# Kernel optimization log

Hardware: AMD Instinct MI355X
Metric: run time of the kernel (lower is better)

The kernel has to match this reference:

```python
import jax, jax.numpy as jnp
import numpy as np

H = 100; W = 100; FX = 86.6; FY = 86.6
NEAR = 2.0; FAR = 6.0; DINF = 1e10
NS = 64            # n_samples per ray
L_PTS = 10; L_DIR = 4
HID = 256; HID_DIR = 128
D_PTS = 3 + 3 * 2 * L_PTS   # 63
D_DIR = 3 + 3 * 2 * L_DIR   # 27


def posenc(x, L):
    # [x, sin(2^k x), cos(2^k x)] NeRF positional encoding
    freqs = (2.0 ** jnp.arange(L)).astype(x.dtype)          # [L]
    xb = x[..., None, :] * freqs[:, None]                    # [..., L, 3]
    enc = jnp.concatenate([jnp.sin(xb), jnp.cos(xb)], -1)    # [..., L, 6]
    return jnp.concatenate([x, enc.reshape(x.shape[:-1] + (L * 6,))], -1)


def setup_inputs() -> dict:
    key = jax.random.key(0)
    ks = jax.random.split(key, 8)
    pose = jnp.array([[1., 0., 0., 0.], [0., 1., 0., 0.],
                      [0., 0., 1., 4.], [0., 0., 0., 1.]], jnp.float32)
    c2w = pose + 0.01 * jax.random.normal(ks[0], (4, 4), jnp.float32)
    t_rand = jax.random.uniform(ks[1], (NS,), jnp.float32)
    s = 0.05
    return {
        'c2w': c2w,
        't_rand': t_rand,
        'w1': s * jax.random.normal(ks[2], (D_PTS, HID), jnp.float32),
        'b1': jnp.zeros((HID,), jnp.float32),
        'w2': s * jax.random.normal(ks[3], (HID, HID), jnp.float32),
        'b2': jnp.zeros((HID,), jnp.float32),
        'w_sig': s * jax.random.normal(ks[4], (HID, 1), jnp.float32),
        'b_sig': jnp.zeros((1,), jnp.float32),
        'w_dir': s * jax.random.normal(ks[5], (HID + D_DIR, HID_DIR), jnp.float32),
        'b_dir': jnp.zeros((HID_DIR,), jnp.float32),
        'w_rgb': s * jax.random.normal(ks[6], (HID_DIR, 3), jnp.float32),
        'b_rgb': jnp.zeros((3,), jnp.float32),
    }


def reference(c2w, t_rand, w1, b1, w2, b2, w_sig, b_sig, w_dir, b_dir, w_rgb, b_rgb):
    # ---- get_rays ----
    i, j = jnp.meshgrid(jnp.arange(W, dtype=jnp.float32),
                        jnp.arange(H, dtype=jnp.float32), indexing='xy')
    dirs = jnp.stack([(i - W * 0.5) / FX,
                      -(j - H * 0.5) / FY,
                      -jnp.ones_like(i)], -1).reshape(H * W, 3)      # [R,3]
    rays_d = jnp.einsum('rk,ik->ri', dirs, c2w[:3, :3])              # [R,3]
    rays_o = c2w[:3, -1]                                             # [3]

    # ---- sample_stratified (perturb=True, inverse_depth=False) ----
    t_vals = jnp.linspace(0.0, 1.0, NS)
    z = NEAR * (1.0 - t_vals) + FAR * t_vals
    mids = 0.5 * (z[1:] + z[:-1])
    upper = jnp.concatenate([mids, z[-1:]])
    lower = jnp.concatenate([z[:1], mids])
    z = lower + (upper - lower) * t_rand                             # [NS]
    dists = jnp.concatenate([z[1:] - z[:-1], jnp.full((1,), DINF, z.dtype)])
    pts = rays_o + rays_d[:, None, :] * z[None, :, None]             # [R,NS,3]

    # ---- encodings ----
    enc_pts = posenc(pts, L_PTS)                                     # [R,NS,63]
    norm = jnp.sqrt(jnp.sum(rays_d * rays_d, -1, keepdims=True))     # [R,1]
    viewdirs = rays_d / norm                                         # [R,3]
    enc_dir = jnp.broadcast_to(posenc(viewdirs, L_DIR)[:, None, :],
                               (H * W, NS, D_DIR))                   # [R,NS,27]

    # ---- coarse NeRF MLP ----
    h = jax.nn.relu(enc_pts @ w1 + b1)
    h = jax.nn.relu(h @ w2 + b2)
    sigma = (h @ w_sig + b_sig)[..., 0]                              # [R,NS]
    hd = jax.nn.relu(jnp.concatenate([h, enc_dir], -1) @ w_dir + b_dir)
    rgb = jax.nn.sigmoid(hd @ w_rgb + b_rgb)                         # [R,NS,3]

    # ---- raw2outputs (volume rendering) ----
    dists_r = dists[None, :] * norm                                  # [R,NS]
    alpha = 1.0 - jnp.exp(-jax.nn.relu(sigma) * dists_r)             # [R,NS]
    # get_rgb_map back-to-front recurrence == alpha * exclusive_cumprod(1-alpha)
    trans = jnp.concatenate(
        [jnp.ones_like(alpha[:, :1]), jnp.cumprod(1.0 - alpha, -1)[:, :-1]], -1)
    weights = alpha * trans                                          # [R,NS]
    rgb_map = jnp.sum(weights[..., None] * rgb, -2)                  # [R,3]
    return rgb_map
```

## Files before the change

### kernel.cpp

```cpp
#include <hip/hip_runtime.h>
#include <cstdint>
#include <cmath>

#define NTH 256

namespace {

typedef _Float16 half8  __attribute__((ext_vector_type(8)));
typedef _Float16 half4v __attribute__((ext_vector_type(4)));
typedef float    float4v __attribute__((ext_vector_type(4)));

constexpr int IMG_W   = 100;
constexpr int NS      = 64;
constexpr int D_PTS   = 63;
constexpr int D_DIR   = 27;
constexpr int HID     = 256;
constexpr int HID_DIR = 128;

constexpr int ENC_H = 72;
constexpr int H_S   = 260;
constexpr int HD_S  = 132;

constexpr int W1P_OFF  = 0;
constexpr int W2P_OFF  = 16384;
constexpr int WDP_OFF  = 81920;
constexpr int WRGB_OFF = 123392;
constexpr int WPACK_HALFS = 125440;

__global__ __launch_bounds__(NTH)
void prepack(const float* __restrict__ w1, const float* __restrict__ w2,
             const float* __restrict__ wd, const float* __restrict__ wsig,
             const float* __restrict__ wrgb, _Float16* __restrict__ wp)
{
    const int idx = blockIdx.x * NTH + threadIdx.x;
    if (idx >= WPACK_HALFS) return;
    const int j    = idx & 7;
    const int lane = (idx >> 3) & 63;
    const int kloc = (lane >> 4) * 8 + j;
    const int lr   = lane & 15;
    float v = 0.0f;
    if (idx < W2P_OFF) {
        const int nt = (idx >> 9) & 15, ks = idx >> 13;
        const int k = ks * 32 + kloc;
        if (k < D_PTS) v = w1[k * HID + nt * 16 + lr];
    } else if (idx < WDP_OFF) {
        const int t = idx - W2P_OFF;
        const int nt = (t >> 9) & 15, ks = t >> 13;
        v = w2[(ks * 32 + kloc) * HID + nt * 16 + lr];
    } else if (idx < WRGB_OFF) {
        const int t = idx - WDP_OFF;
        const int q = t >> 9;
        const int ks = q / 9, tile = q - 9 * ks;
        const int k = ks * 32 + kloc;
        if (tile < 8) { if (k < HID + D_DIR) v = wd[k * HID_DIR + tile * 16 + lr]; }
        else if (lr == 0 && k < HID) v = wsig[k];
    } else {
        const int t = idx - WRGB_OFF;
        const int ks = t >> 9;
        const int k = ks * 32 + kloc;
        if (lr < 3) v = wrgb[k * 3 + lr];
    }
    wp[idx] = (_Float16)v;
}

__device__ __forceinline__ half8 bf_w(const float* __restrict__ W, int ldN,
                                      int kbase, int n, int kmax) {
    half8 b;
    #pragma unroll
    for (int j = 0; j < 8; ++j) {
        const int k = kbase + j;
        b[j] = (_Float16)((k < kmax) ? W[k * ldN + n] : 0.0f);
    }
    return b;
}
__device__ __forceinline__ half8 bf_sig(const float* __restrict__ ws, int kbase, int lr) {
    half8 b;
    #pragma unroll
    for (int j = 0; j < 8; ++j)
        b[j] = (_Float16)((lr == 0) ? ws[kbase + j] : 0.0f);
    return b;
}
__device__ __forceinline__ half8 bf_rgb(const float* __restrict__ wr, int kbase, int lr) {
    half8 b;
    #pragma unroll
    for (int j = 0; j < 8; ++j)
        b[j] = (_Float16)((lr < 3) ? wr[(kbase + j) * 3 + lr] : 0.0f);
    return b;
}

__device__ __forceinline__ half8 ld_h8(const _Float16* __restrict__ p) {
    const half4v lo = *reinterpret_cast<const half4v*>(p);
    const half4v hi = *reinterpret_cast<const half4v*>(p + 4);
    return __builtin_shufflevector(lo, hi, 0, 1, 2, 3, 4, 5, 6, 7);
}

__device__ __forceinline__ double z_of(int s, const float* __restrict__ t_rand) {
    const double delta = 1.0 / 63.0;
    const double ts = (s == 63) ? 1.0 : (double)s * delta;
    const double zs = 2.0 * (1.0 - ts) + 6.0 * ts;
    double lower, upper;
    if (s == 0) { lower = zs; }
    else { const double tm = (double)(s - 1) * delta;
           const double zm = 2.0 * (1.0 - tm) + 6.0 * tm; lower = 0.5 * (zm + zs); }
    if (s == 63) { upper = zs; }
    else { const double tp = (s + 1 == 63) ? 1.0 : (double)(s + 1) * delta;
           const double zp = 2.0 * (1.0 - tp) + 6.0 * tp; upper = 0.5 * (zs + zp); }
    return lower + (upper - lower) * (double)t_rand[s];
}

template<bool PACKED>
__global__ __launch_bounds__(NTH, 4)
void nerf_fused(const float* __restrict__ c2w,
                const float* __restrict__ t_rand,
                const float* __restrict__ w1,  const float* __restrict__ b1,
                const float* __restrict__ w2,  const float* __restrict__ b2,
                const float* __restrict__ w_sig, const float* __restrict__ b_sig,
                const float* __restrict__ w_dir, const float* __restrict__ b_dir,
                const float* __restrict__ w_rgb, const float* __restrict__ b_rgb,
                const _Float16* __restrict__ wpack,
                float* __restrict__ out)
{
    __shared__ __align__(16) unsigned char scr[NS * H_S * 2];
    _Float16* encH = reinterpret_cast<_Float16*>(scr);
    _Float16* hbuf = reinterpret_cast<_Float16*>(scr);
    double*   encD = reinterpret_cast<double*>(scr);
    double*   h1d  = reinterpret_cast<double*>(scr + 512);
    double*   h2d  = reinterpret_cast<double*>(scr + 2560);
    __shared__ __align__(16) _Float16 encdirH[32];
    __shared__ float  sigb[NS];
    __shared__ float  rgbb[NS * 3];

    const int tid  = threadIdx.x;
    const int ray  = blockIdx.x;
    const int lane = tid & 63;
    const int wv   = tid >> 6;
    const int lr   = lane & 15;
    const int lq   = lane >> 4;

    const half8* wp8 = reinterpret_cast<const half8*>(wpack);

    const int pj = ray / IMG_W;
    const int pi = ray - pj * IMG_W;
    const float dx = ((float)pi - 50.0f) / 86.6f;
    const float dy = -(((float)pj) - 50.0f) / 86.6f;
    const float rd0 = dx * c2w[0] + dy * c2w[1] - c2w[2];
    const float rd1 = dx * c2w[4] + dy * c2w[5] - c2w[6];
    const float rd2 = dx * c2w[8] + dy * c2w[9] - c2w[10];
    const float ro0 = c2w[3], ro1 = c2w[7], ro2 = c2w[11];
    const float nrm = sqrtf(rd0 * rd0 + rd1 * rd1 + rd2 * rd2);
    const float vd0 = rd0 / nrm, vd1 = rd1 / nrm, vd2 = rd2 / nrm;

    if (tid < 192) {
        const int s = tid / 3;
        const int c = tid - 3 * s;
        const float zv = (float)z_of(s, t_rand);
        const float p = (c == 0) ? (ro0 + rd0 * zv) : ((c == 1) ? (ro1 + rd1 * zv) : (ro2 + rd2 * zv));
        _Float16* row = &encH[s * ENC_H];
        row[c] = (_Float16)p;
        float sl = sinf(p), cl = cosf(p);
        row[3 + c] = (_Float16)sl;
        row[6 + c] = (_Float16)cl;
        #pragma unroll
        for (int l = 1; l < 10; ++l) {
            const float s2 = 2.0f * sl * cl;
            const float c2 = 1.0f - 2.0f * sl * sl;
            row[3 + 6 * l + c]     = (_Float16)s2;
            row[3 + 6 * l + 3 + c] = (_Float16)c2;
            sl = s2; cl = c2;
        }
    } else if (tid < 224) {
        const int f = tid - 192;
        float v = 0.0f;
        if (f < D_DIR) {
            if (f < 3) {
                v = (f == 0) ? vd0 : ((f == 1) ? vd1 : vd2);
            } else {
                const int ff = f - 3;
                const int l = ff / 6;
                const int r = ff - 6 * l;
                const int c = r % 3;
                const float x = ((c == 0) ? vd0 : ((c == 1) ? vd1 : vd2)) * (float)(1 << l);
                v = (r < 3) ? sinf(x) : cosf(x);
            }
        }
        encdirH[f] = (_Float16)v;
    }
    if (tid < 64) encH[tid * ENC_H + 63] = (_Float16)0.0f;
    __syncthreads();

    {
        float4v acc[4][4];
        #pragma unroll
        for (int nt = 0; nt < 4; ++nt) {
            const float4v bb = *reinterpret_cast<const float4v*>(&b1[(wv * 4 + nt) * 16 + lq * 4]);
            #pragma unroll
            for (int st = 0; st < 4; ++st) acc[nt][st] = bb;
        }

        #pragma unroll
        for (int ks = 0; ks < 2; ++ks) {
            half8 h[4];
            #pragma unroll
            for (int st = 0; st < 4; ++st)
                h[st] = *reinterpret_cast<const half8*>(&encH[(st * 16 + lr) * ENC_H + ks * 32 + lq * 8]);
            __builtin_amdgcn_s_setprio(1);
            #pragma unroll
            for (int nt = 0; nt < 4; ++nt) {
                const int tile = wv * 4 + nt;
                const half8 w = PACKED
                    ? wp8[(W1P_OFF >> 3) + (ks * 16 + tile) * 64 + lane]
                    : bf_w(w1, HID, ks * 32 + lq * 8, tile * 16 + lr, D_PTS);
                #pragma unroll
                for (int st = 0; st < 4; ++st)
                    acc[nt][st] = __builtin_amdgcn_mfma_f32_16x16x32_f16(w, h[st], acc[nt][st], 0, 0, 0);
            }
            __builtin_amdgcn_s_setprio(0);
        }
        __syncthreads();
        #pragma unroll
        for (int nt = 0; nt < 4; ++nt) {
            const int nb = (wv * 4 + nt) * 16 + lq * 4;
            #pragma unroll
            for (int st = 0; st < 4; ++st) {
                half4v hv;
                #pragma unroll
                for (int r = 0; r < 4; ++r)
                    hv[r] = (_Float16)fmaxf(acc[nt][st][r], 0.0f);
                *reinterpret_cast<half4v*>(&hbuf[(st * 16 + lr) * H_S + nb]) = hv;
            }
        }
    }
    __syncthreads();

    {
        float4v acc[4][4];
        #pragma unroll
        for (int nt = 0; nt < 4; ++nt) {
            const float4v bb = *reinterpret_cast<const float4v*>(&b2[(wv * 4 + nt) * 16 + lq * 4]);
            #pragma unroll
            for (int st = 0; st < 4; ++st) acc[nt][st] = bb;
        }

        for (int ks = 0; ks < 8; ++ks) {
            half8 h[4];
            #pragma unroll
            for (int st = 0; st < 4; ++st)
                h[st] = ld_h8(&hbuf[(st * 16 + lr) * H_S + ks * 32 + lq * 8]);
            __builtin_amdgcn_s_setprio(1);
            #pragma unroll
            for (int nt = 0; nt < 4; ++nt) {
                const int tile = wv * 4 + nt;
                const half8 w = PACKED
                    ? wp8[(W2P_OFF >> 3) + (ks * 16 + tile) * 64 + lane]
                    : bf_w(w2, HID, ks * 32 + lq * 8, tile * 16 + lr, 1 << 30);
                #pragma unroll
                for (int st = 0; st < 4; ++st)
                    acc[nt][st] = __builtin_amdgcn_mfma_f32_16x16x32_f16(w, h[st], acc[nt][st], 0, 0, 0);
            }
            __builtin_amdgcn_s_setprio(0);
        }
        __syncthreads();
        #pragma unroll
        for (int nt = 0; nt < 4; ++nt) {
            const int nb = (wv * 4 + nt) * 16 + lq * 4;
            #pragma unroll
            for (int st = 0; st < 4; ++st) {
                half4v hv;
                #pragma unroll
                for (int r = 0; r < 4; ++r)
                    hv[r] = (_Float16)fmaxf(acc[nt][st][r], 0.0f);
                *reinterpret_cast<half4v*>(&hbuf[(st * 16 + lr) * H_S + nb]) = hv;
            }
        }
    }
    __syncthreads();

    float4v accd[2][4];
    float4v accs[4];
    {
        #pragma unroll
        for (int nt = 0; nt < 2; ++nt) {
            const float4v bb = *reinterpret_cast<const float4v*>(&b_dir[(wv * 2 + nt) * 16 + lq * 4]);
            #pragma unroll
            for (int st = 0; st < 4; ++st) accd[nt][st] = bb;
        }
        #pragma unroll
        for (int st = 0; st < 4; ++st) accs[st] = float4v{0.f, 0.f, 0.f, 0.f};

        for (int ks = 0; ks < 8; ++ks) {
            half8 h[4];
            #pragma unroll
            for (int st = 0; st < 4; ++st)
                h[st] = ld_h8(&hbuf[(st * 16 + lr) * H_S + ks * 32 + lq * 8]);
            __builtin_amdgcn_s_setprio(1);
            #pragma unroll
            for (int nt = 0; nt < 2; ++nt) {
                const int tile = wv * 2 + nt;
                const half8 w = PACKED
                    ? wp8[(WDP_OFF >> 3) + (ks * 9 + tile) * 64 + lane]
                    : bf_w(w_dir, HID_DIR, ks * 32 + lq * 8, tile * 16 + lr, 1 << 30);
                #pragma unroll
                for (int st = 0; st < 4; ++st)
                    accd[nt][st] = __builtin_amdgcn_mfma_f32_16x16x32_f16(w, h[st], accd[nt][st], 0, 0, 0);
            }
            if (wv == 0) {
                const half8 w = PACKED
                    ? wp8[(WDP_OFF >> 3) + (ks * 9 + 8) * 64 + lane]
                    : bf_sig(w_sig, ks * 32 + lq * 8, lr);
                #pragma unroll
                for (int st = 0; st < 4; ++st)
                    accs[st] = __builtin_amdgcn_mfma_f32_16x16x32_f16(w, h[st], accs[st], 0, 0, 0);
            }
            __builtin_amdgcn_s_setprio(0);
        }
        {
            const half8 he = *reinterpret_cast<const half8*>(&encdirH[lq * 8]);
            __builtin_amdgcn_s_setprio(1);
            #pragma unroll
            for (int nt = 0; nt < 2; ++nt) {
                const int tile = wv * 2 + nt;
                const half8 w = PACKED
                    ? wp8[(WDP_OFF >> 3) + (8 * 9 + tile) * 64 + lane]
                    : bf_w(w_dir, HID_DIR, HID + lq * 8, tile * 16 + lr, HID + D_DIR);
                #pragma unroll
                for (int st = 0; st < 4; ++st)
                    accd[nt][st] = __builtin_amdgcn_mfma_f32_16x16x32_f16(w, he, accd[nt][st], 0, 0, 0);
            }
            __builtin_amdgcn_s_setprio(0);
        }
    }
    __syncthreads();

    #pragma unroll
    for (int nt = 0; nt < 2; ++nt) {
        const int nb = (wv * 2 + nt) * 16 + lq * 4;
        #pragma unroll
        for (int st = 0; st < 4; ++st) {
            half4v hv;
            #pragma unroll
            for (int r = 0; r < 4; ++r)
                hv[r] = (_Float16)fmaxf(accd[nt][st][r], 0.0f);
            *reinterpret_cast<half4v*>(&hbuf[(st * 16 + lr) * HD_S + nb]) = hv;
        }
    }
    if (wv == 0 && lq == 0) {
        const float bs = b_sig[0];
        #pragma unroll
        for (int st = 0; st < 4; ++st)
            sigb[st * 16 + lr] = accs[st][0] + bs;
    }
    __syncthreads();

    {
        float4v accr = float4v{0.f, 0.f, 0.f, 0.f};
        __builtin_amdgcn_s_setprio(1);
        #pragma unroll
        for (int ks = 0; ks < 4; ++ks) {
            const half8 h = ld_h8(&hbuf[(wv * 16 + lr) * HD_S + ks * 32 + lq * 8]);
            const half8 w = PACKED
                ? wp8[(WRGB_OFF >> 3) + ks * 64 + lane]
                : bf_rgb(w_rgb, ks * 32 + lq * 8, lr);
            accr = __builtin_amdgcn_mfma_f32_16x16x32_f16(w, h, accr, 0, 0, 0);
        }
        __builtin_amdgcn_s_setprio(0);
        if (lq == 0) {
            #pragma unroll
            for (int r = 0; r < 3; ++r) {
                const float a = accr[r] + b_rgb[r];
                rgbb[(wv * 16 + lr) * 3 + r] = 1.0f / (1.0f + expf(-a));
            }
        }
    }
    __syncthreads();

    if (fabsf(sigb[63]) < 0.02f) {
        {
            const double z63 = z_of(63, t_rand);
            const double p0 = (double)ro0 + (double)rd0 * z63;
            const double p1 = (double)ro1 + (double)rd1 * z63;
            const double p2 = (double)ro2 + (double)rd2 * z63;
            if (tid < D_PTS) {
                const int f = tid;
                double v;
                if (f < 3) {
                    v = (f == 0) ? p0 : ((f == 1) ? p1 : p2);
                } else {
                    const int ff = f - 3;
                    const int l = ff / 6;
                    const int r = ff - 6 * l;
                    const int c = r % 3;
                    const double x = ((c == 0) ? p0 : ((c == 1) ? p1 : p2)) * (double)(1 << l);
                    v = (r < 3) ? sin(x) : cos(x);
                }
                encD[f] = v;
            }
        }
        __syncthreads();
        {
            double a0 = 0.0, a1 = 0.0, a2 = 0.0, a3 = 0.0;
            int k = 0;
            for (; k + 4 <= 60; k += 4) {
                a0 += encD[k]     * (double)w1[(k)     * HID + tid];
                a1 += encD[k + 1] * (double)w1[(k + 1) * HID + tid];
                a2 += encD[k + 2] * (double)w1[(k + 2) * HID + tid];
                a3 += encD[k + 3] * (double)w1[(k + 3) * HID + tid];
            }
            a0 += encD[60] * (double)w1[60 * HID + tid];
            a1 += encD[61] * (double)w1[61 * HID + tid];
            a2 += encD[62] * (double)w1[62 * HID + tid];
            const double acc = ((a0 + a1) + (a2 + a3)) + (double)b1[tid];
            h1d[tid] = fmax(acc, 0.0);
        }
        __syncthreads();
        {
            double a0 = 0.0, a1 = 0.0, a2 = 0.0, a3 = 0.0;
            for (int k = 0; k < HID; k += 4) {
                a0 += h1d[k]     * (double)w2[(k)     * HID + tid];
                a1 += h1d[k + 1] * (double)w2[(k + 1) * HID + tid];
                a2 += h1d[k + 2] * (double)w2[(k + 2) * HID + tid];
                a3 += h1d[k + 3] * (double)w2[(k + 3) * HID + tid];
            }
            const double acc = ((a0 + a1) + (a2 + a3)) + (double)b2[tid];
            h2d[tid] = fmax(acc, 0.0);
        }
        __syncthreads();
        if (tid < 64) {
            double p = 0.0;
            #pragma unroll
            for (int m = 0; m < 4; ++m)
                p += h2d[tid * 4 + m] * (double)w_sig[tid * 4 + m];
            #pragma unroll
            for (int off = 1; off < 64; off <<= 1)
                p += __shfl_xor(p, off, 64);
            if (tid == 0) sigb[63] = (float)(p + (double)b_sig[0]);
        }
    }
    __syncthreads();

    if (tid < NS) {
        const int s = tid;
        const float sgv = sigb[s];
        const float zv  = (float)z_of(s, t_rand);
        const float zn  = __shfl_down(zv, 1, 64);
        const float dist = (s < 63) ? (zn - zv) : 1.0e10f;
        const float alpha = 1.0f - expf(-fmaxf(sgv, 0.0f) * dist * nrm);
        float P = 1.0f - alpha;
        #pragma unroll
        for (int off = 1; off < 64; off <<= 1) {
            const float p = __shfl_up(P, off, 64);
            if (s >= off) P *= p;
        }
        float T = __shfl_up(P, 1, 64);
        if (s == 0) T = 1.0f;
        const float wgt = alpha * T;
        float r0 = wgt * rgbb[s * 3 + 0];
        float r1 = wgt * rgbb[s * 3 + 1];
        float r2 = wgt * rgbb[s * 3 + 2];
        #pragma unroll
        for (int off = 32; off > 0; off >>= 1) {
            r0 += __shfl_xor(r0, off, 64);
            r1 += __shfl_xor(r1, off, 64);
            r2 += __shfl_xor(r2, off, 64);
        }
        if (s == 0) {
            out[ray * 3 + 0] = r0;
            out[ray * 3 + 1] = r1;
            out[ray * 3 + 2] = r2;
        }
    }
}

}

extern "C" void kernel_launch(void* const* d_in, const int* in_sizes, int n_in,
                              void* d_out, int out_size, void* d_ws, size_t ws_size,
                              hipStream_t stream) {
    const float* c2w    = (const float*)d_in[0];
    const float* t_rand = (const float*)d_in[1];
    const float* w1     = (const float*)d_in[2];
    const float* b1     = (const float*)d_in[3];
    const float* w2     = (const float*)d_in[4];
    const float* b2     = (const float*)d_in[5];
    const float* w_sig  = (const float*)d_in[6];
    const float* b_sig  = (const float*)d_in[7];
    const float* w_dir  = (const float*)d_in[8];
    const float* b_dir  = (const float*)d_in[9];
    const float* w_rgb  = (const float*)d_in[10];
    const float* b_rgb  = (const float*)d_in[11];

    (void)in_sizes; (void)n_in; (void)out_size;

    const bool packed = (ws_size >= (size_t)(WPACK_HALFS * 2));
    if (packed) {
        _Float16* wp = (_Float16*)d_ws;
        hipLaunchKernelGGL(prepack, dim3((WPACK_HALFS + NTH - 1) / NTH), dim3(NTH), 0, stream,
                           w1, w2, w_dir, w_sig, w_rgb, wp);
        hipLaunchKernelGGL((nerf_fused<true>), dim3(100 * 100), dim3(NTH), 0, stream,
                           c2w, t_rand, w1, b1, w2, b2, w_sig, b_sig,
                           w_dir, b_dir, w_rgb, b_rgb, (const _Float16*)wp, (float*)d_out);
    } else {
        hipLaunchKernelGGL((nerf_fused<false>), dim3(100 * 100), dim3(NTH), 0, stream,
                           c2w, t_rand, w1, b1, w2, b2, w_sig, b_sig,
                           w_dir, b_dir, w_rgb, b_rgb, (const _Float16*)nullptr, (float*)d_out);
    }
}
```

Measured before the change: 277.4 us.

## Give each wave its own sample rows and full output width to drop block barriers

Work is redistributed so each wave owns 16 samples across all 256 (or 128) output columns, instead of all 64 samples over a quarter of the columns. Each wave now builds its own encoding rows in a private LDS region, and the direction encoding is built in registers via shuffles. This removes almost every __syncthreads between MLP layers and the shared encdir buffer. In exchange each wave loads four times as many weight fragments from global/L2 (no reuse across sample tiles), and the accumulator arrays grow, which raises register pressure.

```diff
diff --git a/kernel.cpp b/kernel.cpp
--- a/kernel.cpp
+++ b/kernel.cpp
@@ -17,7 +17,8 @@
 constexpr int HID     = 256;
 constexpr int HID_DIR = 128;
 
-constexpr int ENC_H = 72;
+constexpr int REG_H = 4160;
+constexpr int ENC_S = 72;
 constexpr int H_S   = 260;
 constexpr int HD_S  = 132;
 
@@ -120,13 +121,10 @@
                 const _Float16* __restrict__ wpack,
                 float* __restrict__ out)
 {
-    __shared__ __align__(16) unsigned char scr[NS * H_S * 2];
-    _Float16* encH = reinterpret_cast<_Float16*>(scr);
-    _Float16* hbuf = reinterpret_cast<_Float16*>(scr);
+    __shared__ __align__(16) unsigned char scr[4 * REG_H * 2];
     double*   encD = reinterpret_cast<double*>(scr);
     double*   h1d  = reinterpret_cast<double*>(scr + 512);
     double*   h2d  = reinterpret_cast<double*>(scr + 2560);
-    __shared__ __align__(16) _Float16 encdirH[32];
     __shared__ float  sigb[NS];
     __shared__ float  rgbb[NS * 3];
 
@@ -137,6 +135,7 @@
     const int lr   = lane & 15;
     const int lq   = lane >> 4;
 
+    _Float16* myR = reinterpret_cast<_Float16*>(scr) + wv * REG_H;
     const half8* wp8 = reinterpret_cast<const half8*>(wpack);
 
     const int pj = ray / IMG_W;
@@ -150,213 +149,161 @@
     const float nrm = sqrtf(rd0 * rd0 + rd1 * rd1 + rd2 * rd2);
     const float vd0 = rd0 / nrm, vd1 = rd1 / nrm, vd2 = rd2 / nrm;
 
-    if (tid < 192) {
-        const int s = tid / 3;
-        const int c = tid - 3 * s;
-        const float zv = (float)z_of(s, t_rand);
-        const float p = (c == 0) ? (ro0 + rd0 * zv) : ((c == 1) ? (ro1 + rd1 * zv) : (ro2 + rd2 * zv));
-        _Float16* row = &encH[s * ENC_H];
-        row[c] = (_Float16)p;
-        float sl = sinf(p), cl = cosf(p);
-        row[3 + c] = (_Float16)sl;
-        row[6 + c] = (_Float16)cl;
-        #pragma unroll
-        for (int l = 1; l < 10; ++l) {
-            const float s2 = 2.0f * sl * cl;
-            const float c2 = 1.0f - 2.0f * sl * sl;
-            row[3 + 6 * l + c]     = (_Float16)s2;
-            row[3 + 6 * l + 3 + c] = (_Float16)c2;
-            sl = s2; cl = c2;
-        }
-    } else if (tid < 224) {
-        const int f = tid - 192;
-        float v = 0.0f;
-        if (f < D_DIR) {
+    {
+        const int s = (wv << 4) + lr;
+        if (lq < 3) {
+            const int c = lq;
+            const float zv = (float)z_of(s, t_rand);
+            const float p = (c == 0) ? (ro0 + rd0 * zv) : ((c == 1) ? (ro1 + rd1 * zv) : (ro2 + rd2 * zv));
+            _Float16* row = &myR[lr * ENC_S];
+            row[c] = (_Float16)p;
+            float sl = sinf(p), cl = cosf(p);
+            row[3 + c] = (_Float16)sl;
+            row[6 + c] = (_Float16)cl;
+            #pragma unroll
+            for (int l = 1; l < 10; ++l) {
+                const float s2 = 2.0f * sl * cl;
+                const float c2 = 1.0f - 2.0f * sl * sl;
+                row[3 + 6 * l + c]     = (_Float16)s2;
+                row[3 + 6 * l + 3 + c] = (_Float16)c2;
+                sl = s2; cl = c2;
+            }
+        } else {
+            myR[lr * ENC_S + 63] = (_Float16)0.0f;
+        }
+    }
+
+    half8 he;
+    {
+        float edv = 0.0f;
+        if (lane < D_DIR) {
+            const int f = lane;
             if (f < 3) {
-                v = (f == 0) ? vd0 : ((f == 1) ? vd1 : vd2);
+                edv = (f == 0) ? vd0 : ((f == 1) ? vd1 : vd2);
             } else {
                 const int ff = f - 3;
                 const int l = ff / 6;
                 const int r = ff - 6 * l;
                 const int c = r % 3;
                 const float x = ((c == 0) ? vd0 : ((c == 1) ? vd1 : vd2)) * (float)(1 << l);
-                v = (r < 3) ? sinf(x) : cosf(x);
-            }
-        }
-        encdirH[f] = (_Float16)v;
-    }
-    if (tid < 64) encH[tid * ENC_H + 63] = (_Float16)0.0f;
-    __syncthreads();
-
-    {
-        float4v acc[4][4];
-        #pragma unroll
-        for (int nt = 0; nt < 4; ++nt) {
-            const float4v bb = *reinterpret_cast<const float4v*>(&b1[(wv * 4 + nt) * 16 + lq * 4]);
-            #pragma unroll
-            for (int st = 0; st < 4; ++st) acc[nt][st] = bb;
-        }
+                edv = (r < 3) ? sinf(x) : cosf(x);
+            }
+        }
+        #pragma unroll
+        for (int j = 0; j < 8; ++j)
+            he[j] = (_Float16)__shfl(edv, lq * 8 + j, 64);
+    }
+
+    {
+        float4v acc[16];
+        #pragma unroll
+        for (int nt = 0; nt < 16; ++nt)
+            acc[nt] = *reinterpret_cast<const float4v*>(&b1[nt * 16 + lq * 4]);
 
         #pragma unroll
         for (int ks = 0; ks < 2; ++ks) {
-            half8 h[4];
-            #pragma unroll
-            for (int st = 0; st < 4; ++st)
-                h[st] = *reinterpret_cast<const half8*>(&encH[(st * 16 + lr) * ENC_H + ks * 32 + lq * 8]);
+            const half8 h = *reinterpret_cast<const half8*>(&myR[lr * ENC_S + ks * 32 + lq * 8]);
             __builtin_amdgcn_s_setprio(1);
             #pragma unroll
-            for (int nt = 0; nt < 4; ++nt) {
-                const int tile = wv * 4 + nt;
+            for (int nt = 0; nt < 16; ++nt) {
                 const half8 w = PACKED
-                    ? wp8[(W1P_OFF >> 3) + (ks * 16 + tile) * 64 + lane]
-                    : bf_w(w1, HID, ks * 32 + lq * 8, tile * 16 + lr, D_PTS);
-                #pragma unroll
-                for (int st = 0; st < 4; ++st)
-                    acc[nt][st] = __builtin_amdgcn_mfma_f32_16x16x32_f16(w, h[st], acc[nt][st], 0, 0, 0);
+                    ? wp8[(W1P_OFF >> 3) + (ks * 16 + nt) * 64 + lane]
+                    : bf_w(w1, HID, ks * 32 + lq * 8, nt * 16 + lr, D_PTS);
+                acc[nt] = __builtin_amdgcn_mfma_f32_16x16x32_f16(w, h, acc[nt], 0, 0, 0);
             }
             __builtin_amdgcn_s_setprio(0);
         }
-        __syncthreads();
-        #pragma unroll
-        for (int nt = 0; nt < 4; ++nt) {
-            const int nb = (wv * 4 + nt) * 16 + lq * 4;
-            #pragma unroll
-            for (int st = 0; st < 4; ++st) {
-                half4v hv;
-                #pragma unroll
-                for (int r = 0; r < 4; ++r)
-                    hv[r] = (_Float16)fmaxf(acc[nt][st][r], 0.0f);
-                *reinterpret_cast<half4v*>(&hbuf[(st * 16 + lr) * H_S + nb]) = hv;
-            }
-        }
-    }
-    __syncthreads();
-
-    {
-        float4v acc[4][4];
-        #pragma unroll
-        for (int nt = 0; nt < 4; ++nt) {
-            const float4v bb = *reinterpret_cast<const float4v*>(&b2[(wv * 4 + nt) * 16 + lq * 4]);
-            #pragma unroll
-            for (int st = 0; st < 4; ++st) acc[nt][st] = bb;
-        }
+        #pragma unroll
+        for (int nt = 0; nt < 16; ++nt) {
+            half4v hv;
+            #pragma unroll
+            for (int r = 0; r < 4; ++r)
+                hv[r] = (_Float16)fmaxf(acc[nt][r], 0.0f);
+            *reinterpret_cast<half4v*>(&myR[lr * H_S + nt * 16 + lq * 4]) = hv;
+        }
+    }
+
+    {
+        float4v acc[16];
+        #pragma unroll
+        for (int nt = 0; nt < 16; ++nt)
+            acc[nt] = *reinterpret_cast<const float4v*>(&b2[nt * 16 + lq * 4]);
 
         for (int ks = 0; ks < 8; ++ks) {
-            half8 h[4];
-            #pragma unroll
-            for (int st = 0; st < 4; ++st)
-                h[st] = ld_h8(&hbuf[(st * 16 + lr) * H_S + ks * 32 + lq * 8]);
+            const half8 h = ld_h8(&myR[lr * H_S + ks * 32 + lq * 8]);
             __builtin_amdgcn_s_setprio(1);
             #pragma unroll
-            for (int nt = 0; nt < 4; ++nt) {
-                const int tile = wv * 4 + nt;
+            for (int nt = 0; nt < 16; ++nt) {
                 const half8 w = PACKED
-                    ? wp8[(W2P_OFF >> 3) + (ks * 16 + tile) * 64 + lane]
-                    : bf_w(w2, HID, ks * 32 + lq * 8, tile * 16 + lr, 1 << 30);
-                #pragma unroll
-                for (int st = 0; st < 4; ++st)
-                    acc[nt][st] = __builtin_amdgcn_mfma_f32_16x16x32_f16(w, h[st], acc[nt][st], 0, 0, 0);
+                    ? wp8[(W2P_OFF >> 3) + (ks * 16 + nt) * 64 + lane]
+                    : bf_w(w2, HID, ks * 32 + lq * 8, nt * 16 + lr, 1 << 30);
+                acc[nt] = __builtin_amdgcn_mfma_f32_16x16x32_f16(w, h, acc[nt], 0, 0, 0);
             }
             __builtin_amdgcn_s_setprio(0);
         }
-        __syncthreads();
-        #pragma unroll
-        for (int nt = 0; nt < 4; ++nt) {
-            const int nb = (wv * 4 + nt) * 16 + lq * 4;
-            #pragma unroll
-            for (int st = 0; st < 4; ++st) {
-                half4v hv;
-                #pragma unroll
-                for (int r = 0; r < 4; ++r)
-                    hv[r] = (_Float16)fmaxf(acc[nt][st][r], 0.0f);
-                *reinterpret_cast<half4v*>(&hbuf[(st * 16 + lr) * H_S + nb]) = hv;
-            }
-        }
-    }
-    __syncthreads();
-
-    float4v accd[2][4];
-    float4v accs[4];
-    {
-        #pragma unroll
-        for (int nt = 0; nt < 2; ++nt) {
-            const float4v bb = *reinterpret_cast<const float4v*>(&b_dir[(wv * 2 + nt) * 16 + lq * 4]);
-            #pragma unroll
-            for (int st = 0; st < 4; ++st) accd[nt][st] = bb;
-        }
-        #pragma unroll
-        for (int st = 0; st < 4; ++st) accs[st] = float4v{0.f, 0.f, 0.f, 0.f};
+        #pragma unroll
+        for (int nt = 0; nt < 16; ++nt) {
+            half4v hv;
+            #pragma unroll
+            for (int r = 0; r < 4; ++r)
+                hv[r] = (_Float16)fmaxf(acc[nt][r], 0.0f);
+            *reinterpret_cast<half4v*>(&myR[lr * H_S + nt * 16 + lq * 4]) = hv;
+        }
+    }
+
+    {
+        float4v accd[8];
+        float4v accs = float4v{0.f, 0.f, 0.f, 0.f};
+        #pragma unroll
+        for (int nt = 0; nt < 8; ++nt)
+            accd[nt] = *reinterpret_cast<const float4v*>(&b_dir[nt * 16 + lq * 4]);
 
         for (int ks = 0; ks < 8; ++ks) {
-            half8 h[4];
-            #pragma unroll
-            for (int st = 0; st < 4; ++st)
-                h[st] = ld_h8(&hbuf[(st * 16 + lr) * H_S + ks * 32 + lq * 8]);
+            const half8 h = ld_h8(&myR[lr * H_S + ks * 32 + lq * 8]);
             __builtin_amdgcn_s_setprio(1);
             #pragma unroll
-            for (int nt = 0; nt < 2; ++nt) {
-                const int tile = wv * 2 + nt;
+            for (int nt = 0; nt < 8; ++nt) {
                 const half8 w = PACKED
-                    ? wp8[(WDP_OFF >> 3) + (ks * 9 + tile) * 64 + lane]
-                    : bf_w(w_dir, HID_DIR, ks * 32 + lq * 8, tile * 16 + lr, 1 << 30);
-                #pragma unroll
-                for (int st = 0; st < 4; ++st)
-                    accd[nt][st] = __builtin_amdgcn_mfma_f32_16x16x32_f16(w, h[st], accd[nt][st], 0, 0, 0);
-            }
-            if (wv == 0) {
+                    ? wp8[(WDP_OFF >> 3) + (ks * 9 + nt) * 64 + lane]
+                    : bf_w(w_dir, HID_DIR, ks * 32 + lq * 8, nt * 16 + lr, 1 << 30);
+                accd[nt] = __builtin_amdgcn_mfma_f32_16x16x32_f16(w, h, accd[nt], 0, 0, 0);
+            }
+            {
                 const half8 w = PACKED
                     ? wp8[(WDP_OFF >> 3) + (ks * 9 + 8) * 64 + lane]
                     : bf_sig(w_sig, ks * 32 + lq * 8, lr);
-                #pragma unroll
-                for (int st = 0; st < 4; ++st)
-                    accs[st] = __builtin_amdgcn_mfma_f32_16x16x32_f16(w, h[st], accs[st], 0, 0, 0);
+                accs = __builtin_amdgcn_mfma_f32_16x16x32_f16(w, h, accs, 0, 0, 0);
             }
             __builtin_amdgcn_s_setprio(0);
         }
-        {
-            const half8 he = *reinterpret_cast<const half8*>(&encdirH[lq * 8]);
-            __builtin_amdgcn_s_setprio(1);
-            #pragma unroll
-            for (int nt = 0; nt < 2; ++nt) {
-                const int tile = wv * 2 + nt;
-                const half8 w = PACKED
-                    ? wp8[(WDP_OFF >> 3) + (8 * 9 + tile) * 64 + lane]
-                    : bf_w(w_dir, HID_DIR, HID + lq * 8, tile * 16 + lr, HID + D_DIR);
-                #pragma unroll
-                for (int st = 0; st < 4; ++st)
-                    accd[nt][st] = __builtin_amdgcn_mfma_f32_16x16x32_f16(w, he, accd[nt][st], 0, 0, 0);
-            }
-            __builtin_amdgcn_s_setprio(0);
-        }
-    }
-    __syncthreads();
-
-    #pragma unroll
-    for (int nt = 0; nt < 2; ++nt) {
-        const int nb = (wv * 2 + nt) * 16 + lq * 4;
-        #pragma unroll
-        for (int st = 0; st < 4; ++st) {
+        __builtin_amdgcn_s_setprio(1);
+        #pragma unroll
+        for (int nt = 0; nt < 8; ++nt) {
+            const half8 w = PACKED
+                ? wp8[(WDP_OFF >> 3) + (8 * 9 + nt) * 64 + lane]
+                : bf_w(w_dir, HID_DIR, HID + lq * 8, nt * 16 + lr, HID + D_DIR);
+            accd[nt] = __builtin_amdgcn_mfma_f32_16x16x32_f16(w, he, accd[nt], 0, 0, 0);
+        }
+        __builtin_amdgcn_s_setprio(0);
+
+        #pragma unroll
+        for (int nt = 0; nt < 8; ++nt) {
             half4v hv;
             #pragma unroll
             for (int r = 0; r < 4; ++r)
-                hv[r] = (_Float16)fmaxf(accd[nt][st][r], 0.0f);
-            *reinterpret_cast<half4v*>(&hbuf[(st * 16 + lr) * HD_S + nb]) = hv;
-        }
-    }
-    if (wv == 0 && lq == 0) {
-        const float bs = b_sig[0];
-        #pragma unroll
-        for (int st = 0; st < 4; ++st)
-            sigb[st * 16 + lr] = accs[st][0] + bs;
-    }
-    __syncthreads();
+                hv[r] = (_Float16)fmaxf(accd[nt][r], 0.0f);
+            *reinterpret_cast<half4v*>(&myR[lr * HD_S + nt * 16 + lq * 4]) = hv;
+        }
+        if (lq == 0)
+            sigb[(wv << 4) + lr] = accs[0] + b_sig[0];
+    }
 
     {
         float4v accr = float4v{0.f, 0.f, 0.f, 0.f};
         __builtin_amdgcn_s_setprio(1);
         #pragma unroll
         for (int ks = 0; ks < 4; ++ks) {
-            const half8 h = ld_h8(&hbuf[(wv * 16 + lr) * HD_S + ks * 32 + lq * 8]);
+            const half8 h = ld_h8(&myR[lr * HD_S + ks * 32 + lq * 8]);
             const half8 w = PACKED
                 ? wp8[(WRGB_OFF >> 3) + ks * 64 + lane]
                 : bf_rgb(w_rgb, ks * 32 + lq * 8, lr);
@@ -367,7 +314,7 @@
             #pragma unroll
             for (int r = 0; r < 3; ++r) {
                 const float a = accr[r] + b_rgb[r];
-                rgbb[(wv * 16 + lr) * 3 + r] = 1.0f / (1.0f + expf(-a));
+                rgbb[((wv << 4) + lr) * 3 + r] = 1.0f / (1.0f + expf(-a));
             }
         }
     }
```

Result: slower. 433.9 us (+56.4%).
